# Kernel tuning notes

Measured on AMD Instinct MI355X. Metric: run time of the kernel, lower is better.

Reference implementation:

```python
import jax, jax.numpy as jnp
import numpy as np

B, T, D, H, R, N = 16, 1024, 1024, 256, 64, 8


def setup_inputs() -> dict:
    key = jax.random.key(0)
    ks = jax.random.split(key, 8)
    s = lambda k, shape, fan: jax.random.normal(k, shape, jnp.float32) / np.sqrt(fan)
    return {
        "x": jax.random.normal(ks[0], (B, T, D), jnp.float32),
        "W_base": s(ks[1], (D, D), D),
        "b_base": jnp.zeros((D,), jnp.float32),
        "W_enc": s(ks[2], (N, D, H), D),
        "b_enc": jnp.zeros((N, H), jnp.float32),
        "W_dec": s(ks[3], (N, H, D), H),
        "b_dec": jnp.zeros((N, D), jnp.float32),
        "W_down": s(ks[4], (N, D, R), D),
        "b_down": jnp.zeros((N, R), jnp.float32),
        "W_up": s(ks[5], (N, R, D), R),
        "b_up": jnp.zeros((N, D), jnp.float32),
        "connected_idx": jnp.arange(N, dtype=jnp.int32),
    }


def reference(x, W_base, b_base, W_enc, b_enc, W_dec, b_dec,
              W_down, b_down, W_up, b_up, connected_idx):
    # Base layer: Linear(D, D)
    base = jnp.einsum("btd,de->bte", x, W_base) + b_base

    # All discriminators in parallel (stack_module_state + vmap equivalent).
    # Autoencoder reconstruction loss per (discriminator, sample).
    h = jax.nn.relu(jnp.einsum("btd,ndh->nbth", x, W_enc) + b_enc[:, None, None, :])
    recon = jnp.einsum("nbth,nhd->nbtd", h, W_dec) + b_dec[:, None, None, :]
    losses = jnp.mean((recon - x[None]) ** 2, axis=(2, 3))  # [N, B]

    # Per-sample routing: argmin over discriminators -> connected adapter id.
    top1 = jnp.argmin(losses, axis=0)          # [B]
    adp = connected_idx[top1]                  # [B]

    # Gather selected adapter params (stack_module_state of chosen adapters)
    # and apply per-sample (vmap + functional_call equivalent).
    Wd, bd = W_down[adp], b_down[adp]          # [B,D,R], [B,R]
    Wu, bu = W_up[adp], b_up[adp]              # [B,R,D], [B,D]
    mid = jax.nn.relu(jnp.einsum("btd,bdr->btr", x, Wd) + bd[:, None, :])
    adapter_out = jnp.einsum("btr,brd->btd", mid, Wu) + bu[:, None, :]

    return base + adapter_out
```

## Files before the change

kernel.cpp:

```cpp
#include <hip/hip_runtime.h>
#include <stdint.h>

#define B_  16
#define T_  1024
#define D_  1024
#define H_  256
#define R_  64
#define N_  8
#define BT_ (B_ * T_)

typedef unsigned short u16;
typedef __bf16 bf16_t;
typedef bf16_t bf16x8 __attribute__((ext_vector_type(8)));
typedef float f32x4 __attribute__((ext_vector_type(4)));

__device__ __forceinline__ u16 f2bf(float f) {
    union { float f; uint32_t u; } v; v.f = f;
    uint32_t u = v.u;
    u += 0x7FFFu + ((u >> 16) & 1u);
    return (u16)(u >> 16);
}

__device__ __forceinline__ void gl_lds16(const void* g, void* l) {
    __builtin_amdgcn_global_load_lds(
        (const __attribute__((address_space(1))) void*)g,
        (__attribute__((address_space(3))) void*)l, 16, 0, 0);
}


__global__ __launch_bounds__(256) void cvt_x_kernel(const float* __restrict__ in,
                                                    u16* __restrict__ outp, int n4) {
    int i = blockIdx.x * 256 + threadIdx.x;
    if (i >= n4) return;
    float4 v = reinterpret_cast<const float4*>(in)[i];
    ushort4 o;
    o.x = f2bf(v.x); o.y = f2bf(v.y); o.z = f2bf(v.z); o.w = f2bf(v.w);
    reinterpret_cast<ushort4*>(outp)[i] = o;
}

__global__ __launch_bounds__(256) void transpose_cvt_kernel(const float* __restrict__ in,
                                                            u16* __restrict__ outp,
                                                            int Rr, int Cc) {
    __shared__ u16 tile[64][65];
    const size_t zofs = (size_t)blockIdx.z * Rr * Cc;
    const float* src = in + zofs;
    u16* dst = outp + zofs;
    const int r0 = blockIdx.y * 64, c0 = blockIdx.x * 64;
    const int tx = threadIdx.x & 63, ty = threadIdx.x >> 6;
#pragma unroll
    for (int i = 0; i < 16; i++) {
        int r = i * 4 + ty;
        tile[r][tx] = f2bf(src[(size_t)(r0 + r) * Cc + (c0 + tx)]);
    }
    __syncthreads();
#pragma unroll
    for (int i = 0; i < 16; i++) {
        int r = i * 4 + ty;
        dst[(size_t)(c0 + r) * Rr + (r0 + tx)] = tile[tx][r];
    }
}

__global__ __launch_bounds__(256) void enc_loss_kernel(
    const u16* __restrict__ xb, const float* __restrict__ x,
    const u16* __restrict__ Wenc_t,
    const float* __restrict__ b_enc,
    const u16* __restrict__ Wdec_t,
    const float* __restrict__ b_dec,
    float* __restrict__ losses) {

    __shared__ u16 lds_a[64 * 32];
    __shared__ u16 lds_b[256 * 32];
    __shared__ u16 lds_h[64 * 264];
    __shared__ float red[256];

    const int n = blockIdx.y;
    const int r0 = blockIdx.x * 64;
    const int bsamp = r0 >> 10;
    const int t = threadIdx.x;
    const int w = t >> 6;
    const int l = t & 63;
    const int lr = l & 15;
    const int lq = l >> 4;
    const int lk = lq * 8;

    const u16* We = Wenc_t + (size_t)n * H_ * D_;
    const u16* Wd = Wdec_t + (size_t)n * D_ * H_;

    const f32x4 fzero = {0.f, 0.f, 0.f, 0.f};
    f32x4 acc[4][4];
#pragma unroll
    for (int mt = 0; mt < 4; mt++)
#pragma unroll
        for (int nt = 0; nt < 4; nt++) acc[mt][nt] = fzero;

    for (int ks = 0; ks < 32; ks++) {
        const int k0 = ks * 32;
        __syncthreads();
        {
            int c = w * 64 + l, row = c >> 2, kc = c & 3;
            gl_lds16(&xb[(size_t)(r0 + row) * D_ + k0 + kc * 8],
                     (char*)lds_a + w * 1024);
        }
#pragma unroll
        for (int i = 0; i < 4; i++) {
            int j = w * 4 + i;
            int c = j * 64 + l, row = c >> 2, kc = c & 3;
            gl_lds16(&We[(size_t)row * D_ + k0 + kc * 8],
                     (char*)lds_b + j * 1024);
        }
        __syncthreads();
        bf16x8 af[4], bfr[4];
#pragma unroll
        for (int mt = 0; mt < 4; mt++)
            af[mt] = *reinterpret_cast<const bf16x8*>(&lds_a[(mt * 16 + lr) * 32 + lk]);
#pragma unroll
        for (int nt = 0; nt < 4; nt++)
            bfr[nt] = *reinterpret_cast<const bf16x8*>(&lds_b[(w * 64 + nt * 16 + lr) * 32 + lk]);
#pragma unroll
        for (int mt = 0; mt < 4; mt++)
#pragma unroll
            for (int nt = 0; nt < 4; nt++)
                acc[mt][nt] = __builtin_amdgcn_mfma_f32_16x16x32_bf16(af[mt], bfr[nt], acc[mt][nt], 0, 0, 0);
    }
    __syncthreads();
#pragma unroll
    for (int mt = 0; mt < 4; mt++)
#pragma unroll
        for (int nt = 0; nt < 4; nt++) {
            int hc = w * 64 + nt * 16 + lr;
            float bias = b_enc[n * H_ + hc];
#pragma unroll
            for (int r = 0; r < 4; r++) {
                int row = mt * 16 + lq * 4 + r;
                float v2 = acc[mt][nt][r] + bias;
                lds_h[row * 264 + hc] = f2bf(v2 > 0.f ? v2 : 0.f);
            }
        }
    __syncthreads();

    float lacc = 0.f;
    for (int chk = 0; chk < 4; chk++) {
#pragma unroll
        for (int mt = 0; mt < 4; mt++)
#pragma unroll
            for (int nt = 0; nt < 4; nt++) acc[mt][nt] = fzero;
        for (int ks = 0; ks < 8; ks++) {
            __syncthreads();
#pragma unroll
            for (int i = 0; i < 4; i++) {
                int j = w * 4 + i;
                int c = j * 64 + l, row = c >> 2, kc = c & 3;
                gl_lds16(&Wd[(size_t)(chk * 256 + row) * H_ + ks * 32 + kc * 8],
                         (char*)lds_b + j * 1024);
            }
            __syncthreads();
            bf16x8 af[4], bfr[4];
#pragma unroll
            for (int mt = 0; mt < 4; mt++)
                af[mt] = *reinterpret_cast<const bf16x8*>(&lds_h[(mt * 16 + lr) * 264 + ks * 32 + lk]);
#pragma unroll
            for (int nt = 0; nt < 4; nt++)
                bfr[nt] = *reinterpret_cast<const bf16x8*>(&lds_b[(w * 64 + nt * 16 + lr) * 32 + lk]);
#pragma unroll
            for (int mt = 0; mt < 4; mt++)
#pragma unroll
                for (int nt = 0; nt < 4; nt++)
                    acc[mt][nt] = __builtin_amdgcn_mfma_f32_16x16x32_bf16(af[mt], bfr[nt], acc[mt][nt], 0, 0, 0);
        }
#pragma unroll
        for (int mt = 0; mt < 4; mt++)
#pragma unroll
            for (int nt = 0; nt < 4; nt++) {
                int d = chk * 256 + w * 64 + nt * 16 + lr;
                float bias = b_dec[n * D_ + d];
#pragma unroll
                for (int r = 0; r < 4; r++) {
                    int row = mt * 16 + lq * 4 + r;
                    float recon = acc[mt][nt][r] + bias;
                    float diff = recon - x[(size_t)(r0 + row) * D_ + d];
                    lacc += diff * diff;
                }
            }
    }

    red[t] = lacc;
    __syncthreads();
    for (int s = 128; s > 0; s >>= 1) {
        if (t < s) red[t] += red[t + s];
        __syncthreads();
    }
    if (t == 0) atomicAdd(&losses[n * B_ + bsamp], red[0]);
}

__global__ void argmin_kernel(const float* __restrict__ losses,
                              const int* __restrict__ cidx,
                              int* __restrict__ adp) {
    int b = threadIdx.x;
    if (b < B_) {
        float best = losses[b];
        int bi = 0;
        for (int n = 1; n < N_; n++) {
            float v = losses[n * B_ + b];
            if (v < best) { best = v; bi = n; }
        }
        adp[b] = cidx[bi];
    }
}

__global__ __launch_bounds__(256) void down_kernel(
    const u16* __restrict__ xb,
    const u16* __restrict__ Wdown_t,
    const float* __restrict__ b_down,
    const int* __restrict__ adp,
    u16* __restrict__ mid) {
    __shared__ char smem[65536];
    const int r0 = blockIdx.x * 64;
    const int n = adp[r0 >> 10];
    const u16* Wd = Wdown_t + (size_t)n * R_ * D_;
    const int t = threadIdx.x, w = t >> 6, l = t & 63;
    const int lr = l & 15, lq = l >> 4, lk = lq * 8;
    char* wbase = smem + w * 8192;
    const u16* sa = (const u16*)wbase;
    const u16* sb = (const u16*)(wbase + 4096);
    const f32x4 fzero = {0.f, 0.f, 0.f, 0.f};
    f32x4 acc[4][4];
#pragma unroll
    for (int mt = 0; mt < 4; mt++)
#pragma unroll
        for (int nt = 0; nt < 4; nt++) acc[mt][nt] = fzero;

    for (int ks2 = 0; ks2 < 8; ks2++) {
        const int k0 = (w * 8 + ks2) * 32;
        __syncthreads();
#pragma unroll
        for (int i = 0; i < 4; i++) {
            int c = i * 64 + l, row = c >> 2, kc = c & 3;
            gl_lds16(&xb[(size_t)(r0 + row) * D_ + k0 + kc * 8], wbase + i * 1024);
            gl_lds16(&Wd[(size_t)row * D_ + k0 + kc * 8], wbase + 4096 + i * 1024);
        }
        __syncthreads();
        bf16x8 af[4], bfr[4];
#pragma unroll
        for (int mt = 0; mt < 4; mt++)
            af[mt] = *reinterpret_cast<const bf16x8*>(&sa[(mt * 16 + lr) * 32 + lk]);
#pragma unroll
        for (int nt = 0; nt < 4; nt++)
            bfr[nt] = *reinterpret_cast<const bf16x8*>(&sb[(nt * 16 + lr) * 32 + lk]);
#pragma unroll
        for (int mt = 0; mt < 4; mt++)
#pragma unroll
            for (int nt = 0; nt < 4; nt++)
                acc[mt][nt] = __builtin_amdgcn_mfma_f32_16x16x32_bf16(af[mt], bfr[nt], acc[mt][nt], 0, 0, 0);
    }

    __syncthreads();
    float* pr = (float*)smem;
#pragma unroll
    for (int mt = 0; mt < 4; mt++)
#pragma unroll
        for (int nt = 0; nt < 4; nt++)
#pragma unroll
            for (int r = 0; r < 4; r++)
                pr[w * 4096 + (mt * 16 + lq * 4 + r) * 64 + nt * 16 + lr] = acc[mt][nt][r];
    __syncthreads();
#pragma unroll
    for (int ei = 0; ei < 16; ei++) {
        int e = ei * 256 + t;
        float s = pr[e] + pr[4096 + e] + pr[8192 + e] + pr[12288 + e];
        int row = e >> 6, col = e & 63;
        float v = s + b_down[n * R_ + col];
        mid[(size_t)(r0 + row) * R_ + col] = f2bf(v > 0.f ? v : 0.f);
    }
}

__global__ __launch_bounds__(256) void out_kernel(
    const u16* __restrict__ xb,
    const u16* __restrict__ Wb_t,
    const float* __restrict__ b_base,
    const u16* __restrict__ mid,
    const u16* __restrict__ Wup_t,
    const float* __restrict__ b_up,
    const int* __restrict__ adp,
    float* __restrict__ outp) {
    __shared__ u16 lds_a[128 * 32];
    __shared__ u16 lds_b[128 * 32];
    const int c0 = blockIdx.x * 128;
    const int r0 = blockIdx.y * 128;
    const int n = adp[r0 >> 10];
    const int t = threadIdx.x, w = t >> 6, l = t & 63;
    const int wm = (w >> 1) * 64, wn = (w & 1) * 64;
    const int lr = l & 15, lq = l >> 4, lk = lq * 8;
    const f32x4 fzero = {0.f, 0.f, 0.f, 0.f};
    f32x4 acc[4][4];
#pragma unroll
    for (int mt = 0; mt < 4; mt++)
#pragma unroll
        for (int nt = 0; nt < 4; nt++) acc[mt][nt] = fzero;

    for (int ks = 0; ks < 32; ks++) {
        const int k0 = ks * 32;
        __syncthreads();
#pragma unroll
        for (int i = 0; i < 2; i++) {
            int j = w * 2 + i;
            int c = j * 64 + l, row = c >> 2, kc = c & 3;
            gl_lds16(&xb[(size_t)(r0 + row) * D_ + k0 + kc * 8],
                     (char*)lds_a + j * 1024);
            gl_lds16(&Wb_t[(size_t)(c0 + row) * D_ + k0 + kc * 8],
                     (char*)lds_b + j * 1024);
        }
        __syncthreads();
        bf16x8 af[4], bfr[4];
#pragma unroll
        for (int mt = 0; mt < 4; mt++)
            af[mt] = *reinterpret_cast<const bf16x8*>(&lds_a[(wm + mt * 16 + lr) * 32 + lk]);
#pragma unroll
        for (int nt = 0; nt < 4; nt++)
            bfr[nt] = *reinterpret_cast<const bf16x8*>(&lds_b[(wn + nt * 16 + lr) * 32 + lk]);
#pragma unroll
        for (int mt = 0; mt < 4; mt++)
#pragma unroll
            for (int nt = 0; nt < 4; nt++)
                acc[mt][nt] = __builtin_amdgcn_mfma_f32_16x16x32_bf16(af[mt], bfr[nt], acc[mt][nt], 0, 0, 0);
    }

    const u16* Wu = Wup_t + (size_t)n * D_ * R_;
    for (int ks = 0; ks < 2; ks++) {
        const int k0 = ks * 32;
        __syncthreads();
#pragma unroll
        for (int i = 0; i < 2; i++) {
            int j = w * 2 + i;
            int c = j * 64 + l, row = c >> 2, kc = c & 3;
            gl_lds16(&mid[(size_t)(r0 + row) * R_ + k0 + kc * 8],
                     (char*)lds_a + j * 1024);
            gl_lds16(&Wu[(size_t)(c0 + row) * R_ + k0 + kc * 8],
                     (char*)lds_b + j * 1024);
        }
        __syncthreads();
        bf16x8 af[4], bfr[4];
#pragma unroll
        for (int mt = 0; mt < 4; mt++)
            af[mt] = *reinterpret_cast<const bf16x8*>(&lds_a[(wm + mt * 16 + lr) * 32 + lk]);
#pragma unroll
        for (int nt = 0; nt < 4; nt++)
            bfr[nt] = *reinterpret_cast<const bf16x8*>(&lds_b[(wn + nt * 16 + lr) * 32 + lk]);
#pragma unroll
        for (int mt = 0; mt < 4; mt++)
#pragma unroll
            for (int nt = 0; nt < 4; nt++)
                acc[mt][nt] = __builtin_amdgcn_mfma_f32_16x16x32_bf16(af[mt], bfr[nt], acc[mt][nt], 0, 0, 0);
    }

#pragma unroll
    for (int mt = 0; mt < 4; mt++)
#pragma unroll
        for (int nt = 0; nt < 4; nt++) {
            int gc = c0 + wn + nt * 16 + lr;
            float bias = b_base[gc] + b_up[n * D_ + gc];
#pragma unroll
            for (int r = 0; r < 4; r++) {
                int row = r0 + wm + mt * 16 + lq * 4 + r;
                outp[(size_t)row * D_ + gc] = acc[mt][nt][r] + bias;
            }
        }
}

extern "C" void kernel_launch(void* const* d_in, const int* in_sizes, int n_in,
                              void* d_out, int out_size, void* d_ws, size_t ws_size,
                              hipStream_t stream) {
    const float* x      = (const float*)d_in[0];
    const float* W_base = (const float*)d_in[1];
    const float* b_base = (const float*)d_in[2];
    const float* W_enc  = (const float*)d_in[3];
    const float* b_enc  = (const float*)d_in[4];
    const float* W_dec  = (const float*)d_in[5];
    const float* b_dec  = (const float*)d_in[6];
    const float* W_down = (const float*)d_in[7];
    const float* b_down = (const float*)d_in[8];
    const float* W_up   = (const float*)d_in[9];
    const float* b_up   = (const float*)d_in[10];
    const int*   cidx   = (const int*)d_in[11];
    float* outp = (float*)d_out;
    (void)in_sizes; (void)n_in; (void)out_size; (void)ws_size;

    char* p = (char*)d_ws;
    u16* xb      = (u16*)p; p += (size_t)BT_ * D_ * 2;
    u16* Wb_t    = (u16*)p; p += (size_t)D_ * D_ * 2;
    u16* Wenc_t  = (u16*)p; p += (size_t)N_ * H_ * D_ * 2;
    u16* Wdec_t  = (u16*)p; p += (size_t)N_ * D_ * H_ * 2;
    u16* Wdown_t = (u16*)p; p += (size_t)N_ * R_ * D_ * 2;
    u16* Wup_t   = (u16*)p; p += (size_t)N_ * D_ * R_ * 2;
    u16* mid     = (u16*)p; p += (size_t)BT_ * R_ * 2;
    float* losses = (float*)p; p += 256;
    int* adp      = (int*)p; p += 256;

    hipMemsetAsync(losses, 0, N_ * B_ * sizeof(float), stream);

    cvt_x_kernel<<<(BT_ * D_ / 4 + 255) / 256, 256, 0, stream>>>(x, xb, BT_ * D_ / 4);
    transpose_cvt_kernel<<<dim3(D_ / 64, D_ / 64, 1),  256, 0, stream>>>(W_base, Wb_t,    D_, D_);
    transpose_cvt_kernel<<<dim3(H_ / 64, D_ / 64, N_), 256, 0, stream>>>(W_enc,  Wenc_t,  D_, H_);
    transpose_cvt_kernel<<<dim3(D_ / 64, H_ / 64, N_), 256, 0, stream>>>(W_dec,  Wdec_t,  H_, D_);
    transpose_cvt_kernel<<<dim3(R_ / 64, D_ / 64, N_), 256, 0, stream>>>(W_down, Wdown_t, D_, R_);
    transpose_cvt_kernel<<<dim3(D_ / 64, R_ / 64, N_), 256, 0, stream>>>(W_up,   Wup_t,   R_, D_);

    enc_loss_kernel<<<dim3(BT_ / 64, N_), 256, 0, stream>>>(xb, x, Wenc_t, b_enc, Wdec_t, b_dec, losses);
    argmin_kernel<<<1, 64, 0, stream>>>(losses, cidx, adp);
    down_kernel<<<BT_ / 64, 256, 0, stream>>>(xb, Wdown_t, b_down, adp, mid);
    out_kernel<<<dim3(D_ / 128, BT_ / 128), 256, 0, stream>>>(xb, Wb_t, b_base, mid, Wup_t, b_up, adp, outp);
}
```

Baseline: 456.7 us.

## Split encoder/decoder loss into 128x128-tiled GEMMs and merge weight transposes

Replaces the fused encoder+decoder loss kernel, which did a 64-row tile against all of H with weak reuse, with two 128x128-tiled GEMM kernels. The encoder writes the ReLU hidden activations for all 8 discriminators as one wide GEMM into the output buffer as scratch. The decoder kernel loops over discriminators, reading the bf16 x tile once from LDS, and uses wave shuffles instead of an LDS tree for the loss reduction. Five transpose launches are merged into one. In exchange, h (32 MB bf16) makes a round trip through global memory, and the loss now compares against bf16-rounded x instead of fp32 x.

```diff
diff --git a/kernel.cpp b/kernel.cpp
--- a/kernel.cpp
+++ b/kernel.cpp
@@ -8,6 +8,7 @@
 #define R_  64
 #define N_  8
 #define BT_ (B_ * T_)
+#define NH_ (N_ * H_)
 
 typedef unsigned short u16;
 typedef __bf16 bf16_t;
@@ -19,6 +20,9 @@
     uint32_t u = v.u;
     u += 0x7FFFu + ((u >> 16) & 1u);
     return (u16)(u >> 16);
+}
+__device__ __forceinline__ float bf2f(u16 b) {
+    union { float f; uint32_t u; } v; v.u = ((uint32_t)b) << 16; return v.f;
 }
 
 __device__ __forceinline__ void gl_lds16(const void* g, void* l) {
@@ -38,14 +42,35 @@
     reinterpret_cast<ushort4*>(outp)[i] = o;
 }
 
-__global__ __launch_bounds__(256) void transpose_cvt_kernel(const float* __restrict__ in,
-                                                            u16* __restrict__ outp,
-                                                            int Rr, int Cc) {
+__global__ __launch_bounds__(256) void transpose_all_kernel(
+    const float* __restrict__ W_base, u16* __restrict__ Wb_t,
+    const float* __restrict__ W_enc,  u16* __restrict__ Wenc_t,
+    const float* __restrict__ W_dec,  u16* __restrict__ Wdec_t,
+    const float* __restrict__ W_down, u16* __restrict__ Wdown_t,
+    const float* __restrict__ W_up,   u16* __restrict__ Wup_t) {
     __shared__ u16 tile[64][65];
-    const size_t zofs = (size_t)blockIdx.z * Rr * Cc;
-    const float* src = in + zofs;
-    u16* dst = outp + zofs;
-    const int r0 = blockIdx.y * 64, c0 = blockIdx.x * 64;
+    const int b = blockIdx.x;
+    const float* src; u16* dst; int Rr, Cc, xq, yq;
+    if (b < 256) {
+        src = W_base; dst = Wb_t; Rr = D_; Cc = D_; xq = b & 15; yq = b >> 4;
+    } else if (b < 768) {
+        int lcl = b - 256, z = lcl >> 6, rem = lcl & 63;
+        src = W_enc + (size_t)z * D_ * H_; dst = Wenc_t + (size_t)z * H_ * D_;
+        Rr = D_; Cc = H_; xq = rem & 3; yq = rem >> 2;
+    } else if (b < 1280) {
+        int lcl = b - 768, z = lcl >> 6, rem = lcl & 63;
+        src = W_dec + (size_t)z * H_ * D_; dst = Wdec_t + (size_t)z * D_ * H_;
+        Rr = H_; Cc = D_; xq = rem & 15; yq = rem >> 4;
+    } else if (b < 1408) {
+        int lcl = b - 1280, z = lcl >> 4;
+        src = W_down + (size_t)z * D_ * R_; dst = Wdown_t + (size_t)z * R_ * D_;
+        Rr = D_; Cc = R_; xq = 0; yq = lcl & 15;
+    } else {
+        int lcl = b - 1408, z = lcl >> 4;
+        src = W_up + (size_t)z * R_ * D_; dst = Wup_t + (size_t)z * D_ * R_;
+        Rr = R_; Cc = D_; xq = lcl & 15; yq = 0;
+    }
+    const int r0 = yq * 64, c0 = xq * 64;
     const int tx = threadIdx.x & 63, ty = threadIdx.x >> 6;
 #pragma unroll
     for (int i = 0; i < 16; i++) {
@@ -60,136 +85,139 @@
     }
 }
 
-__global__ __launch_bounds__(256) void enc_loss_kernel(
-    const u16* __restrict__ xb, const float* __restrict__ x,
+__global__ __launch_bounds__(256) void enc_kernel(
+    const u16* __restrict__ xb,
     const u16* __restrict__ Wenc_t,
     const float* __restrict__ b_enc,
+    u16* __restrict__ h) {
+    __shared__ u16 lds_a[128 * 32];
+    __shared__ u16 lds_b[128 * 32];
+    const int c0 = blockIdx.x * 128;
+    const int r0 = blockIdx.y * 128;
+    const int t = threadIdx.x, w = t >> 6, l = t & 63;
+    const int wm = (w >> 1) * 64, wn = (w & 1) * 64;
+    const int lr = l & 15, lq = l >> 4, lk = lq * 8;
+    const f32x4 fzero = {0.f, 0.f, 0.f, 0.f};
+    f32x4 acc[4][4];
+#pragma unroll
+    for (int mt = 0; mt < 4; mt++)
+#pragma unroll
+        for (int nt = 0; nt < 4; nt++) acc[mt][nt] = fzero;
+
+    for (int ks = 0; ks < 32; ks++) {
+        const int k0 = ks * 32;
+        __syncthreads();
+#pragma unroll
+        for (int i = 0; i < 2; i++) {
+            int j = w * 2 + i;
+            int c = j * 64 + l, row = c >> 2, kc = c & 3;
+            gl_lds16(&xb[(size_t)(r0 + row) * D_ + k0 + kc * 8], (char*)lds_a + j * 1024);
+            gl_lds16(&Wenc_t[(size_t)(c0 + row) * D_ + k0 + kc * 8], (char*)lds_b + j * 1024);
+        }
+        __syncthreads();
+        bf16x8 af[4], bfr[4];
+#pragma unroll
+        for (int mt = 0; mt < 4; mt++)
+            af[mt] = *reinterpret_cast<const bf16x8*>(&lds_a[(wm + mt * 16 + lr) * 32 + lk]);
+#pragma unroll
+        for (int nt = 0; nt < 4; nt++)
+            bfr[nt] = *reinterpret_cast<const bf16x8*>(&lds_b[(wn + nt * 16 + lr) * 32 + lk]);
+#pragma unroll
+        for (int mt = 0; mt < 4; mt++)
+#pragma unroll
+            for (int nt = 0; nt < 4; nt++)
+                acc[mt][nt] = __builtin_amdgcn_mfma_f32_16x16x32_bf16(af[mt], bfr[nt], acc[mt][nt], 0, 0, 0);
+    }
+#pragma unroll
+    for (int mt = 0; mt < 4; mt++)
+#pragma unroll
+        for (int nt = 0; nt < 4; nt++) {
+            int c = c0 + wn + nt * 16 + lr;
+            float bias = b_enc[c];
+#pragma unroll
+            for (int r = 0; r < 4; r++) {
+                int row = r0 + wm + mt * 16 + lq * 4 + r;
+                float v = acc[mt][nt][r] + bias;
+                h[(size_t)row * NH_ + c] = f2bf(v > 0.f ? v : 0.f);
+            }
+        }
+}
+
+__global__ __launch_bounds__(256) void dec_loss_kernel(
+    const u16* __restrict__ h,
+    const u16* __restrict__ xb,
     const u16* __restrict__ Wdec_t,
     const float* __restrict__ b_dec,
     float* __restrict__ losses) {
-
-    __shared__ u16 lds_a[64 * 32];
-    __shared__ u16 lds_b[256 * 32];
-    __shared__ u16 lds_h[64 * 264];
-    __shared__ float red[256];
-
-    const int n = blockIdx.y;
-    const int r0 = blockIdx.x * 64;
+    __shared__ u16 lds_a[128 * 32];
+    __shared__ u16 lds_b[128 * 32];
+    __shared__ u16 lds_x[128 * 128];
+    const int c0 = blockIdx.x * 128;
+    const int r0 = blockIdx.y * 128;
     const int bsamp = r0 >> 10;
-    const int t = threadIdx.x;
-    const int w = t >> 6;
-    const int l = t & 63;
-    const int lr = l & 15;
-    const int lq = l >> 4;
-    const int lk = lq * 8;
-
-    const u16* We = Wenc_t + (size_t)n * H_ * D_;
-    const u16* Wd = Wdec_t + (size_t)n * D_ * H_;
-
+    const int t = threadIdx.x, w = t >> 6, l = t & 63;
+    const int wm = (w >> 1) * 64, wn = (w & 1) * 64;
+    const int lr = l & 15, lq = l >> 4, lk = lq * 8;
     const f32x4 fzero = {0.f, 0.f, 0.f, 0.f};
-    f32x4 acc[4][4];
-#pragma unroll
-    for (int mt = 0; mt < 4; mt++)
-#pragma unroll
-        for (int nt = 0; nt < 4; nt++) acc[mt][nt] = fzero;
-
-    for (int ks = 0; ks < 32; ks++) {
-        const int k0 = ks * 32;
-        __syncthreads();
-        {
-            int c = w * 64 + l, row = c >> 2, kc = c & 3;
-            gl_lds16(&xb[(size_t)(r0 + row) * D_ + k0 + kc * 8],
-                     (char*)lds_a + w * 1024);
-        }
-#pragma unroll
-        for (int i = 0; i < 4; i++) {
-            int j = w * 4 + i;
-            int c = j * 64 + l, row = c >> 2, kc = c & 3;
-            gl_lds16(&We[(size_t)row * D_ + k0 + kc * 8],
-                     (char*)lds_b + j * 1024);
-        }
-        __syncthreads();
-        bf16x8 af[4], bfr[4];
-#pragma unroll
-        for (int mt = 0; mt < 4; mt++)
-            af[mt] = *reinterpret_cast<const bf16x8*>(&lds_a[(mt * 16 + lr) * 32 + lk]);
-#pragma unroll
-        for (int nt = 0; nt < 4; nt++)
-            bfr[nt] = *reinterpret_cast<const bf16x8*>(&lds_b[(w * 64 + nt * 16 + lr) * 32 + lk]);
-#pragma unroll
-        for (int mt = 0; mt < 4; mt++)
-#pragma unroll
-            for (int nt = 0; nt < 4; nt++)
-                acc[mt][nt] = __builtin_amdgcn_mfma_f32_16x16x32_bf16(af[mt], bfr[nt], acc[mt][nt], 0, 0, 0);
-    }
-    __syncthreads();
-#pragma unroll
-    for (int mt = 0; mt < 4; mt++)
-#pragma unroll
-        for (int nt = 0; nt < 4; nt++) {
-            int hc = w * 64 + nt * 16 + lr;
-            float bias = b_enc[n * H_ + hc];
-#pragma unroll
-            for (int r = 0; r < 4; r++) {
-                int row = mt * 16 + lq * 4 + r;
-                float v2 = acc[mt][nt][r] + bias;
-                lds_h[row * 264 + hc] = f2bf(v2 > 0.f ? v2 : 0.f);
-            }
-        }
-    __syncthreads();
-
-    float lacc = 0.f;
-    for (int chk = 0; chk < 4; chk++) {
+
+#pragma unroll
+    for (int i = 0; i < 8; i++) {
+        int j = w * 8 + i;
+        gl_lds16(&xb[(size_t)(r0 + j * 4 + (l >> 4)) * D_ + c0 + (l & 15) * 8],
+                 (char*)lds_x + j * 1024);
+    }
+
+#pragma unroll 1
+    for (int n = 0; n < N_; n++) {
+        const u16* hn = h + n * H_;
+        const u16* Wd = Wdec_t + (size_t)n * D_ * H_;
+        f32x4 acc[4][4];
 #pragma unroll
         for (int mt = 0; mt < 4; mt++)
 #pragma unroll
             for (int nt = 0; nt < 4; nt++) acc[mt][nt] = fzero;
         for (int ks = 0; ks < 8; ks++) {
+            const int k0 = ks * 32;
             __syncthreads();
 #pragma unroll
-            for (int i = 0; i < 4; i++) {
-                int j = w * 4 + i;
+            for (int i = 0; i < 2; i++) {
+                int j = w * 2 + i;
                 int c = j * 64 + l, row = c >> 2, kc = c & 3;
-                gl_lds16(&Wd[(size_t)(chk * 256 + row) * H_ + ks * 32 + kc * 8],
-                         (char*)lds_b + j * 1024);
+                gl_lds16(&hn[(size_t)(r0 + row) * NH_ + k0 + kc * 8], (char*)lds_a + j * 1024);
+                gl_lds16(&Wd[(size_t)(c0 + row) * H_ + k0 + kc * 8], (char*)lds_b + j * 1024);
             }
             __syncthreads();
             bf16x8 af[4], bfr[4];
 #pragma unroll
             for (int mt = 0; mt < 4; mt++)
-                af[mt] = *reinterpret_cast<const bf16x8*>(&lds_h[(mt * 16 + lr) * 264 + ks * 32 + lk]);
+                af[mt] = *reinterpret_cast<const bf16x8*>(&lds_a[(wm + mt * 16 + lr) * 32 + lk]);
 #pragma unroll
             for (int nt = 0; nt < 4; nt++)
-                bfr[nt] = *reinterpret_cast<const bf16x8*>(&lds_b[(w * 64 + nt * 16 + lr) * 32 + lk]);
+                bfr[nt] = *reinterpret_cast<const bf16x8*>(&lds_b[(wn + nt * 16 + lr) * 32 + lk]);
 #pragma unroll
             for (int mt = 0; mt < 4; mt++)
 #pragma unroll
                 for (int nt = 0; nt < 4; nt++)
                     acc[mt][nt] = __builtin_amdgcn_mfma_f32_16x16x32_bf16(af[mt], bfr[nt], acc[mt][nt], 0, 0, 0);
         }
+        float la = 0.f;
 #pragma unroll
         for (int mt = 0; mt < 4; mt++)
 #pragma unroll
             for (int nt = 0; nt < 4; nt++) {
-                int d = chk * 256 + w * 64 + nt * 16 + lr;
-                float bias = b_dec[n * D_ + d];
+                int col = wn + nt * 16 + lr;
+                float bias = b_dec[n * D_ + c0 + col];
 #pragma unroll
                 for (int r = 0; r < 4; r++) {
-                    int row = mt * 16 + lq * 4 + r;
-                    float recon = acc[mt][nt][r] + bias;
-                    float diff = recon - x[(size_t)(r0 + row) * D_ + d];
-                    lacc += diff * diff;
+                    int row = wm + mt * 16 + lq * 4 + r;
+                    float diff = acc[mt][nt][r] + bias - bf2f(lds_x[row * 128 + col]);
+                    la += diff * diff;
                 }
             }
-    }
-
-    red[t] = lacc;
-    __syncthreads();
-    for (int s = 128; s > 0; s >>= 1) {
-        if (t < s) red[t] += red[t + s];
-        __syncthreads();
-    }
-    if (t == 0) atomicAdd(&losses[n * B_ + bsamp], red[0]);
+#pragma unroll
+        for (int off = 32; off > 0; off >>= 1) la += __shfl_down(la, off, 64);
+        if (l == 0) atomicAdd(&losses[n * B_ + bsamp], la);
+    }
 }
 
 __global__ void argmin_kernel(const float* __restrict__ losses,
@@ -304,10 +332,8 @@
         for (int i = 0; i < 2; i++) {
             int j = w * 2 + i;
             int c = j * 64 + l, row = c >> 2, kc = c & 3;
-            gl_lds16(&xb[(size_t)(r0 + row) * D_ + k0 + kc * 8],
-                     (char*)lds_a + j * 1024);
-            gl_lds16(&Wb_t[(size_t)(c0 + row) * D_ + k0 + kc * 8],
-                     (char*)lds_b + j * 1024);
+            gl_lds16(&xb[(size_t)(r0 + row) * D_ + k0 + kc * 8], (char*)lds_a + j * 1024);
+            gl_lds16(&Wb_t[(size_t)(c0 + row) * D_ + k0 + kc * 8], (char*)lds_b + j * 1024);
         }
         __syncthreads();
         bf16x8 af[4], bfr[4];
@@ -332,10 +358,8 @@
         for (int i = 0; i < 2; i++) {
             int j = w * 2 + i;
             int c = j * 64 + l, row = c >> 2, kc = c & 3;
-            gl_lds16(&mid[(size_t)(r0 + row) * R_ + k0 + kc * 8],
-                     (char*)lds_a + j * 1024);
-            gl_lds16(&Wu[(size_t)(c0 + row) * R_ + k0 + kc * 8],
-                     (char*)lds_b + j * 1024);
+            gl_lds16(&mid[(size_t)(r0 + row) * R_ + k0 + kc * 8], (char*)lds_a + j * 1024);
+            gl_lds16(&Wu[(size_t)(c0 + row) * R_ + k0 + kc * 8], (char*)lds_b + j * 1024);
         }
         __syncthreads();
         bf16x8 af[4], bfr[4];
@@ -395,16 +419,17 @@
     float* losses = (float*)p; p += 256;
     int* adp      = (int*)p; p += 256;
 
+    u16* h = (u16*)d_out;
+
     hipMemsetAsync(losses, 0, N_ * B_ * sizeof(float), stream);
 
     cvt_x_kernel<<<(BT_ * D_ / 4 + 255) / 256, 256, 0, stream>>>(x, xb, BT_ * D_ / 4);
-    transpose_cvt_kernel<<<dim3(D_ / 64, D_ / 64, 1),  256, 0, stream>>>(W_base, Wb_t,    D_, D_);
-    transpose_cvt_kernel<<<dim3(H_ / 64, D_ / 64, N_), 256, 0, stream>>>(W_enc,  Wenc_t,  D_, H_);
-    transpose_cvt_kernel<<<dim3(D_ / 64, H_ / 64, N_), 256, 0, stream>>>(W_dec,  Wdec_t,  H_, D_);
-    transpose_cvt_kernel<<<dim3(R_ / 64, D_ / 64, N_), 256, 0, stream>>>(W_down, Wdown_t, D_, R_);
-    transpose_cvt_kernel<<<dim3(D_ / 64, R_ / 64, N_), 256, 0, stream>>>(W_up,   Wup_t,   R_, D_);
-
-    enc_loss_kernel<<<dim3(BT_ / 64, N_), 256, 0, stream>>>(xb, x, Wenc_t, b_enc, Wdec_t, b_dec, losses);
+    transpose_all_kernel<<<1536, 256, 0, stream>>>(W_base, Wb_t, W_enc, Wenc_t,
+                                                   W_dec, Wdec_t, W_down, Wdown_t,
+                                                   W_up, Wup_t);
+
+    enc_kernel<<<dim3(NH_ / 128, BT_ / 128), 256, 0, stream>>>(xb, Wenc_t, b_enc, h);
+    dec_loss_kernel<<<dim3(D_ / 128, BT_ / 128), 256, 0, stream>>>(h, xb, Wdec_t, b_dec, losses);
     argmin_kernel<<<1, 64, 0, stream>>>(losses, cidx, adp);
     down_kernel<<<BT_ / 64, 256, 0, stream>>>(xb, Wdown_t, b_down, adp, mid);
     out_kernel<<<dim3(D_ / 128, BT_ / 128), 256, 0, stream>>>(xb, Wb_t, b_base, mid, Wup_t, b_up, adp, outp);
```

After: 587.1 us. 28.6% more time.
